# Kernel tuning notes

Hardware: AMD Instinct MI355X
Metric: run time of the kernel (lower is better)

The kernel has to match this reference:

```python
import jax, jax.numpy as jnp
import numpy as np

B, C, OUT, K, H, W = 16, 128, 128, 3, 128, 128
EPS = 1e-5


def setup_inputs() -> dict:
    key = jax.random.key(0)
    ks = jax.random.split(key, 16)
    s = 0.05  # weight init scale to keep activations tame
    d = {
        "ir_feat": jax.random.normal(ks[0], (B, C, H, W), jnp.float32),
        "vi_feat": jax.random.normal(ks[1], (B, C, H, W), jnp.float32),
        # kernel_gen: 1x1 convs on pooled [B,2C,1,1] -> matmuls
        "kg_w1": jax.random.normal(ks[2], (C // 2, 2 * C), jnp.float32) * s,
        "kg_b1": jax.random.normal(ks[3], (C // 2,), jnp.float32) * s,
        "kg_w2": jax.random.normal(ks[4], (OUT * C * K * K, C // 2), jnp.float32) * s,
        "kg_b2": jax.random.normal(ks[5], (OUT * C * K * K,), jnp.float32) * s,
        # bias_gen
        "bg_w1": jax.random.normal(ks[6], (C // 4, 2 * C), jnp.float32) * s,
        "bg_b1": jax.random.normal(ks[7], (C // 4,), jnp.float32) * s,
        "bg_w2": jax.random.normal(ks[8], (OUT, C // 4), jnp.float32) * s,
        "bg_b2": jax.random.normal(ks[9], (OUT,), jnp.float32) * s,
        # enhance: 1x1 conv (no bias) + BN (eval-mode running stats)
        "en_w": jax.random.normal(ks[10], (C, 2 * C), jnp.float32) * s,
        "bn_gamma": jnp.ones((C,), jnp.float32),
        "bn_beta": jnp.zeros((C,), jnp.float32),
        "bn_mean": jax.random.normal(ks[11], (C,), jnp.float32) * 0.1,
        "bn_var": jax.random.uniform(ks[12], (C,), jnp.float32, 0.5, 1.5),
    }
    return d


def reference(ir_feat, vi_feat, kg_w1, kg_b1, kg_w2, kg_b2,
              bg_w1, bg_b1, bg_w2, bg_b2, en_w,
              bn_gamma, bn_beta, bn_mean, bn_var):
    concat = jnp.concatenate([ir_feat, vi_feat], axis=1)        # [B,2C,H,W]
    pooled = concat.mean(axis=(2, 3))                            # AdaptiveAvgPool2d(1) -> [B,2C]

    # dynamic kernel generation (1x1 convs on 1x1 spatial == matmuls)
    hk = jax.nn.relu(pooled @ kg_w1.T + kg_b1)                   # [B,C/2]
    dyn_k = (hk @ kg_w2.T + kg_b2).reshape(B, OUT, C, K, K)      # per-sample conv weights
    hb = jax.nn.relu(pooled @ bg_w1.T + bg_b1)                   # [B,C/4]
    dyn_b = hb @ bg_w2.T + bg_b2                                 # [B,OUT]

    # enhance: 1x1 conv -> BN(eval) -> ReLU
    enh = jnp.einsum('bchw,oc->bohw', concat, en_w)              # [B,C,H,W]
    inv = (bn_gamma / jnp.sqrt(bn_var + EPS))[:, None, None]
    enh = jax.nn.relu(enh * inv + (bn_beta - bn_mean * bn_gamma / jnp.sqrt(bn_var + EPS))[:, None, None])

    # per-sample dynamic conv2d, batched via vmap (replaces the python loop)
    def conv_one(x, w, b):  # x:[C,H,W], w:[OUT,C,K,K], b:[OUT]
        y = jax.lax.conv_general_dilated(
            x[None], w, window_strides=(1, 1), padding=[(1, 1), (1, 1)],
            dimension_numbers=('NCHW', 'OIHW', 'NCHW'))[0]
        return y + b[:, None, None]

    return jax.vmap(conv_one)(enh, dyn_k, dyn_b)                 # [B,OUT,H,W]
```

## Files before the change

kernel.cpp:

```cpp
#include <hip/hip_runtime.h>
#include <hip/hip_bf16.h>

#define B_    16
#define C_    128
#define TWOC  256
#define OUT_  128
#define HW    16384
#define WDIM  128
#define HDIM  128
#define KTOT  1152

typedef __attribute__((ext_vector_type(8))) short short8;
typedef __attribute__((ext_vector_type(4))) float floatx4;

__device__ __forceinline__ ushort f2bf(float f) {
    union { float f; uint u; } x; x.f = f;
    uint r = (x.u + 0x7FFFu + ((x.u >> 16) & 1u)) >> 16;
    return (ushort)r;
}
__device__ __forceinline__ float bf2f(ushort u) {
    union { float f; uint u; } x; x.u = ((uint)u) << 16;
    return x.f;
}
__device__ __forceinline__ uint cvt_pk_bf16(float lo, float hi) {
    uint r;
    asm("v_cvt_pk_bf16_f32 %0, %1, %2" : "=v"(r) : "v"(lo), "v"(hi));
    return r;
}

__global__ __launch_bounds__(256) void prep_kernel(
    const float* __restrict__ en_w, ushort* __restrict__ en_w_bf,
    float* __restrict__ pooled)
{
    int i = blockIdx.x * 256 + threadIdx.x;
    en_w_bf[i] = f2bf(en_w[i]);
    if (i < B_ * TWOC) pooled[i] = 0.f;
}

__global__ __launch_bounds__(256) void enhance_kernel(
    const float* __restrict__ ir, const float* __restrict__ vi,
    const ushort* __restrict__ en_w_bf,
    const float* __restrict__ gamma, const float* __restrict__ beta,
    const float* __restrict__ mean, const float* __restrict__ var,
    ushort* __restrict__ enh, float* __restrict__ pooled)
{
    __shared__ ushort Xs[128][40];
    __shared__ float red[256];
    const int b = blockIdx.y;
    const int p0 = blockIdx.x * 128;
    const int t = threadIdx.x;
    const int lane = t & 63, wave = t >> 6;
    const int wr = wave >> 1, wc = wave & 1;
    const int lr = lane & 15, kg = lane >> 4;
    const int px = t & 127, half = t >> 7;
    const int pc = t & 31, grp = t >> 5;

    floatx4 acc[4][4] = {};
    float fcur[16], fnxt[16];
    short8 a_cur[4], a_nxt[4];

    {
        const float* src = ir + ((size_t)b * C_ + half * 16) * HW + p0 + px;
        #pragma unroll
        for (int jj = 0; jj < 16; ++jj) fcur[jj] = src[(size_t)jj * HW];
        #pragma unroll
        for (int i2 = 0; i2 < 4; ++i2) {
            int co = wr * 64 + i2 * 16 + lr;
            a_cur[i2] = *(const short8*)&en_w_bf[(size_t)co * TWOC + kg * 8];
        }
    }

    #pragma unroll
    for (int kc = 0; kc < 8; ++kc) {
        __syncthreads();
        {
            uint u[8];
            #pragma unroll
            for (int jj = 0; jj < 8; ++jj)
                u[jj] = cvt_pk_bf16(fcur[2 * jj], fcur[2 * jj + 1]);
            uint4* dst = (uint4*)&Xs[px][half * 16];
            dst[0] = make_uint4(u[0], u[1], u[2], u[3]);
            dst[1] = make_uint4(u[4], u[5], u[6], u[7]);
        }
        if (kc > 0 && t < 32) {
            float s = red[t] + red[32 + t] + red[64 + t] + red[96 + t]
                    + red[128 + t] + red[160 + t] + red[192 + t] + red[224 + t];
            atomicAdd(&pooled[b * TWOC + (kc - 1) * 32 + t], s);
        }
        __syncthreads();

        if (kc < 7) {
            int c2b = (kc + 1) * 32 + half * 16;
            const float* src = (c2b < C_)
                ? ir + ((size_t)b * C_ + c2b) * HW + p0 + px
                : vi + ((size_t)b * C_ + (c2b - C_)) * HW + p0 + px;
            #pragma unroll
            for (int jj = 0; jj < 16; ++jj) fnxt[jj] = src[(size_t)jj * HW];
            #pragma unroll
            for (int i2 = 0; i2 < 4; ++i2) {
                int co = wr * 64 + i2 * 16 + lr;
                a_nxt[i2] = *(const short8*)&en_w_bf[(size_t)co * TWOC + (kc + 1) * 32 + kg * 8];
            }
        }

        short8 bfr[4];
        #pragma unroll
        for (int j = 0; j < 4; ++j) {
            int pl = wc * 64 + j * 16 + lr;
            bfr[j] = *(const short8*)&Xs[pl][kg * 8];
        }
        #pragma unroll
        for (int i2 = 0; i2 < 4; ++i2)
            #pragma unroll
            for (int j = 0; j < 4; ++j)
                acc[i2][j] = __builtin_amdgcn_mfma_f32_16x16x32_bf16(a_cur[i2], bfr[j], acc[i2][j], 0, 0, 0);

        {
            float s = 0.f;
            #pragma unroll
            for (int q = 0; q < 16; ++q) s += bf2f(Xs[grp * 16 + q][pc]);
            red[t] = s;
        }

        if (kc < 7) {
            #pragma unroll
            for (int jj = 0; jj < 16; ++jj) fcur[jj] = fnxt[jj];
            #pragma unroll
            for (int i2 = 0; i2 < 4; ++i2) a_cur[i2] = a_nxt[i2];
        }
    }

    __syncthreads();
    if (t < 32) {
        float s = red[t] + red[32 + t] + red[64 + t] + red[96 + t]
                + red[128 + t] + red[160 + t] + red[192 + t] + red[224 + t];
        atomicAdd(&pooled[b * TWOC + 7 * 32 + t], s);
    }

    #pragma unroll
    for (int i2 = 0; i2 < 4; ++i2) {
        int co_b = wr * 64 + i2 * 16 + kg * 4;
        float4 g  = *(const float4*)&gamma[co_b];
        float4 vv = *(const float4*)&var[co_b];
        float4 bt = *(const float4*)&beta[co_b];
        float4 mn = *(const float4*)&mean[co_b];
        float inv0 = g.x * rsqrtf(vv.x + 1e-5f), inv1 = g.y * rsqrtf(vv.y + 1e-5f);
        float inv2 = g.z * rsqrtf(vv.z + 1e-5f), inv3 = g.w * rsqrtf(vv.w + 1e-5f);
        float ad0 = bt.x - mn.x * inv0, ad1 = bt.y - mn.y * inv1;
        float ad2 = bt.z - mn.z * inv2, ad3 = bt.w - mn.w * inv3;
        #pragma unroll
        for (int j = 0; j < 4; ++j) {
            int pl = wc * 64 + j * 16 + lr;
            float v0 = fmaxf(acc[i2][j][0] * inv0 + ad0, 0.f);
            float v1 = fmaxf(acc[i2][j][1] * inv1 + ad1, 0.f);
            float v2 = fmaxf(acc[i2][j][2] * inv2 + ad2, 0.f);
            float v3 = fmaxf(acc[i2][j][3] * inv3 + ad3, 0.f);
            uint2 pk;
            pk.x = cvt_pk_bf16(v0, v1);
            pk.y = cvt_pk_bf16(v2, v3);
            *(uint2*)&enh[((size_t)b * HW + p0 + pl) * C_ + co_b] = pk;
        }
    }
}

__global__ __launch_bounds__(256) void gen_mlp1_kernel(
    const float* __restrict__ pooled,
    const float* __restrict__ kg_w1, const float* __restrict__ kg_b1,
    const float* __restrict__ bg_w1, const float* __restrict__ bg_b1,
    float* __restrict__ hk, float* __restrict__ hb)
{
    const float scale = 1.0f / (float)HW;
    int idx = blockIdx.x * 256 + threadIdx.x;
    if (idx < B_ * 64) {
        int b = idx >> 6, j = idx & 63;
        const float4* w = (const float4*)(kg_w1 + (size_t)j * TWOC);
        const float4* p = (const float4*)(pooled + b * TWOC);
        float s = 0.f;
        #pragma unroll 8
        for (int q = 0; q < 64; ++q) {
            float4 wv = w[q], pv = p[q];
            s += (wv.x * pv.x + wv.y * pv.y) + (wv.z * pv.z + wv.w * pv.w);
        }
        hk[idx] = fmaxf(kg_b1[j] + s * scale, 0.f);
    } else if (idx < B_ * 64 + B_ * 32) {
        int e = idx - B_ * 64;
        int b = e >> 5, j = e & 31;
        const float4* w = (const float4*)(bg_w1 + (size_t)j * TWOC);
        const float4* p = (const float4*)(pooled + b * TWOC);
        float s = 0.f;
        #pragma unroll 8
        for (int q = 0; q < 64; ++q) {
            float4 wv = w[q], pv = p[q];
            s += (wv.x * pv.x + wv.y * pv.y) + (wv.z * pv.z + wv.w * pv.w);
        }
        hb[e] = fmaxf(bg_b1[j] + s * scale, 0.f);
    }
}

__global__ __launch_bounds__(256) void gen_dynk_kernel(
    const float* __restrict__ kg_w2, const float* __restrict__ kg_b2,
    const float* __restrict__ hk, const float* __restrict__ hb,
    const float* __restrict__ bg_w2, const float* __restrict__ bg_b2,
    ushort* __restrict__ dynk, float* __restrict__ dyn_b)
{
    __shared__ float hk_s[B_][64];
    int t = threadIdx.x;
    for (int i = t; i < B_ * 64; i += 256) hk_s[i >> 6][i & 63] = hk[i];
    __syncthreads();

    int i = blockIdx.x * 256 + t;
    int kk = i >> 14;
    int o  = (i >> 7) & 127;
    int c  = i & 127;
    int r  = o * KTOT + c * 9 + kk;

    float wrow[64];
    const float4* w4 = (const float4*)(kg_w2 + (size_t)r * 64);
    #pragma unroll
    for (int q = 0; q < 16; ++q) {
        float4 v = w4[q];
        wrow[4 * q + 0] = v.x; wrow[4 * q + 1] = v.y;
        wrow[4 * q + 2] = v.z; wrow[4 * q + 3] = v.w;
    }
    float bias = kg_b2[r];
    #pragma unroll
    for (int b = 0; b < B_; ++b) {
        float s = bias;
        #pragma unroll
        for (int k2 = 0; k2 < 64; ++k2) s += hk_s[b][k2] * wrow[k2];
        dynk[((size_t)(b * 9 + kk) * 128 + o) * 128 + c] = f2bf(s);
    }

    if (blockIdx.x == 0) {
        for (int e = t; e < B_ * OUT_; e += 256) {
            int b = e >> 7, o2 = e & 127;
            float s = bg_b2[o2];
            const float* w = bg_w2 + o2 * 32;
            const float* h = hb + b * 32;
            #pragma unroll
            for (int k2 = 0; k2 < 32; ++k2) s += h[k2] * w[k2];
            dyn_b[e] = s;
        }
    }
}

__global__ __launch_bounds__(256, 3) void dynconv_kernel(
    const ushort* __restrict__ enh, const ushort* __restrict__ dynk,
    const float* __restrict__ dyn_b, float* __restrict__ out)
{
    __shared__ ushort halo[180][72];
    const int b = blockIdx.z;
    const int gy0 = blockIdx.y * 8, gx0 = blockIdx.x * 16;
    const int t = threadIdx.x, lane = t & 63, wave = t >> 6;
    const int wr = wave >> 1, wc = wave & 1;
    const int lr = lane & 15, kg = lane >> 4;
    const ushort* dynk_b = dynk + (size_t)b * 9 * 128 * 128;
    const ushort* enh_b  = enh + (size_t)b * HW * C_;

    floatx4 acc[4][4] = {};
    short8 a_cur[8], a_nxt[8];

    for (int h = 0; h < 2; ++h) {
        uint4 hreg[6];
        #pragma unroll
        for (int s = 0; s < 6; ++s) {
            int seg = s * 256 + t;
            int hp = seg >> 3, c8 = seg & 7;
            uint4 v = make_uint4(0, 0, 0, 0);
            if (hp < 180) {
                int hy = hp / 18, hx = hp - hy * 18;
                int gy = gy0 - 1 + hy, gx = gx0 - 1 + hx;
                if ((unsigned)gy < 128u && (unsigned)gx < 128u)
                    v = *(const uint4*)&enh_b[((size_t)(gy * WDIM + gx)) * C_ + h * 64 + c8 * 8];
            }
            hreg[s] = v;
        }
        #pragma unroll
        for (int q = 0; q < 8; ++q) {
            int ks = q >> 2, i2 = q & 3;
            int o = wr * 64 + i2 * 16 + lr;
            a_cur[q] = *(const short8*)&dynk_b[(size_t)(0 * 128 + o) * 128 + h * 64 + ks * 32 + kg * 8];
        }
        __syncthreads();
        #pragma unroll
        for (int s = 0; s < 6; ++s) {
            int seg = s * 256 + t;
            int hp = seg >> 3, c8 = seg & 7;
            if (hp < 180) *(uint4*)&halo[hp][c8 * 8] = hreg[s];
        }
        __syncthreads();

        #pragma unroll
        for (int kk = 0; kk < 9; ++kk) {
            if (kk < 8) {
                #pragma unroll
                for (int q = 0; q < 8; ++q) {
                    int ks = q >> 2, i2 = q & 3;
                    int o = wr * 64 + i2 * 16 + lr;
                    a_nxt[q] = *(const short8*)&dynk_b[(size_t)((kk + 1) * 128 + o) * 128 + h * 64 + ks * 32 + kg * 8];
                }
            }
            const int kh = kk / 3, kw = kk - kh * 3;
            #pragma unroll
            for (int ks = 0; ks < 2; ++ks) {
                short8 bfr[4];
                #pragma unroll
                for (int j = 0; j < 4; ++j) {
                    int p = wc * 64 + j * 16 + lr;
                    int py = p >> 4, px = p & 15;
                    bfr[j] = *(const short8*)&halo[(py + kh) * 18 + (px + kw)][ks * 32 + kg * 8];
                }
                #pragma unroll
                for (int i2 = 0; i2 < 4; ++i2)
                    #pragma unroll
                    for (int j = 0; j < 4; ++j)
                        acc[i2][j] = __builtin_amdgcn_mfma_f32_16x16x32_bf16(a_cur[ks * 4 + i2], bfr[j], acc[i2][j], 0, 0, 0);
            }
            #pragma unroll
            for (int q = 0; q < 8; ++q) a_cur[q] = a_nxt[q];
        }
    }

    #pragma unroll
    for (int i2 = 0; i2 < 4; ++i2) {
        int o_b = wr * 64 + i2 * 16 + kg * 4;
        float4 db = *(const float4*)&dyn_b[b * OUT_ + o_b];
        float dbv[4] = {db.x, db.y, db.z, db.w};
        #pragma unroll
        for (int j = 0; j < 4; ++j) {
            int p = wc * 64 + j * 16 + lr;
            int py = p >> 4, px = p & 15;
            int gy = gy0 + py, gx = gx0 + px;
            #pragma unroll
            for (int r = 0; r < 4; ++r) {
                int o = o_b + r;
                out[((size_t)(b * OUT_ + o)) * HW + gy * WDIM + gx] = acc[i2][j][r] + dbv[r];
            }
        }
    }
}

extern "C" void kernel_launch(void* const* d_in, const int* in_sizes, int n_in,
                              void* d_out, int out_size, void* d_ws, size_t ws_size,
                              hipStream_t stream)
{
    const float* ir    = (const float*)d_in[0];
    const float* vi    = (const float*)d_in[1];
    const float* kg_w1 = (const float*)d_in[2];
    const float* kg_b1 = (const float*)d_in[3];
    const float* kg_w2 = (const float*)d_in[4];
    const float* kg_b2 = (const float*)d_in[5];
    const float* bg_w1 = (const float*)d_in[6];
    const float* bg_b1 = (const float*)d_in[7];
    const float* bg_w2 = (const float*)d_in[8];
    const float* bg_b2 = (const float*)d_in[9];
    const float* en_w  = (const float*)d_in[10];
    const float* bn_g  = (const float*)d_in[11];
    const float* bn_b  = (const float*)d_in[12];
    const float* bn_m  = (const float*)d_in[13];
    const float* bn_v  = (const float*)d_in[14];
    float* out = (float*)d_out;

    char* ws = (char*)d_ws;
    float*  pooled = (float*)(ws + 0);
    float*  dyn_b  = (float*)(ws + 16384);
    float*  hk     = (float*)(ws + 24576);
    float*  hb     = (float*)(ws + 28672);
    ushort* dynk   = (ushort*)(ws + 32768);
    ushort* enh    = (ushort*)(ws + 32768 + 4718592);

    size_t en_off = 32768 + 4718592 + 67108864;
    ushort* en_w_bf = (ws_size >= en_off + 65536)
                    ? (ushort*)(ws + en_off)
                    : (ushort*)((char*)d_out + (size_t)out_size - 65536);

    prep_kernel<<<128, 256, 0, stream>>>(en_w, en_w_bf, pooled);
    enhance_kernel<<<dim3(HDIM, B_), 256, 0, stream>>>(ir, vi, en_w_bf, bn_g, bn_b,
                                                       bn_m, bn_v, enh, pooled);
    gen_mlp1_kernel<<<6, 256, 0, stream>>>(pooled, kg_w1, kg_b1, bg_w1, bg_b1, hk, hb);
    gen_dynk_kernel<<<576, 256, 0, stream>>>(kg_w2, kg_b2, hk, hb, bg_w2, bg_b2, dynk, dyn_b);
    dynconv_kernel<<<dim3(WDIM / 16, HDIM / 8, B_), 256, 0, stream>>>(enh, dynk, dyn_b, out);
}
```

Measured before the change: 590.5 us.

## Retile dynamic conv into 4x32 pixel tiles, split output channels across blocks

Changes the dynamic-conv tiling from 8x16 pixels times 128 outputs per block to 4x32 pixels times 64 outputs, so each wave handles one row of 32 pixels. The grid becomes a flat 4096 blocks with an XCD-aware swizzle that groups blocks of the same batch together, and occupancy is raised to 4 blocks per CU by halving the accumulators. The output stores now cover 32 contiguous x-positions per wave, which should coalesce better. In exchange, each halo tile is loaded twice, once for each output half, and weight fragments are reused over fewer pixels.

```diff
diff --git a/kernel.cpp b/kernel.cpp
--- a/kernel.cpp
+++ b/kernel.cpp
@@ -244,31 +244,42 @@
     }
 }
 
-__global__ __launch_bounds__(256, 3) void dynconv_kernel(
+#define TY_   4
+#define TX_   32
+#define HX_   34
+#define NPX_  204
+
+__global__ __launch_bounds__(256, 4) void dynconv_kernel(
     const ushort* __restrict__ enh, const ushort* __restrict__ dynk,
     const float* __restrict__ dyn_b, float* __restrict__ out)
 {
-    __shared__ ushort halo[180][72];
-    const int b = blockIdx.z;
-    const int gy0 = blockIdx.y * 8, gx0 = blockIdx.x * 16;
-    const int t = threadIdx.x, lane = t & 63, wave = t >> 6;
-    const int wr = wave >> 1, wc = wave & 1;
+    __shared__ ushort halo[NPX_][72];
+    const int pid = blockIdx.x;
+    const int lid = (pid & 7) * 512 + (pid >> 3);
+    const int b   = lid >> 8;
+    const int rem = lid & 255;
+    const int oh  = rem & 1;
+    const int tile = rem >> 1;
+    const int ty = tile >> 2, tx = tile & 3;
+    const int gy0 = ty * TY_, gx0 = tx * TX_;
+
+    const int t = threadIdx.x, lane = t & 63, wc = t >> 6;
     const int lr = lane & 15, kg = lane >> 4;
     const ushort* dynk_b = dynk + (size_t)b * 9 * 128 * 128;
     const ushort* enh_b  = enh + (size_t)b * HW * C_;
 
-    floatx4 acc[4][4] = {};
+    floatx4 acc[4][2] = {};
     short8 a_cur[8], a_nxt[8];
 
     for (int h = 0; h < 2; ++h) {
-        uint4 hreg[6];
-        #pragma unroll
-        for (int s = 0; s < 6; ++s) {
+        uint4 hreg[7];
+        #pragma unroll
+        for (int s = 0; s < 7; ++s) {
             int seg = s * 256 + t;
             int hp = seg >> 3, c8 = seg & 7;
             uint4 v = make_uint4(0, 0, 0, 0);
-            if (hp < 180) {
-                int hy = hp / 18, hx = hp - hy * 18;
+            if (hp < NPX_) {
+                int hy = hp / HX_, hx = hp - hy * HX_;
                 int gy = gy0 - 1 + hy, gx = gx0 - 1 + hx;
                 if ((unsigned)gy < 128u && (unsigned)gx < 128u)
                     v = *(const uint4*)&enh_b[((size_t)(gy * WDIM + gx)) * C_ + h * 64 + c8 * 8];
@@ -278,15 +289,15 @@
         #pragma unroll
         for (int q = 0; q < 8; ++q) {
             int ks = q >> 2, i2 = q & 3;
-            int o = wr * 64 + i2 * 16 + lr;
+            int o = oh * 64 + i2 * 16 + lr;
             a_cur[q] = *(const short8*)&dynk_b[(size_t)(0 * 128 + o) * 128 + h * 64 + ks * 32 + kg * 8];
         }
         __syncthreads();
         #pragma unroll
-        for (int s = 0; s < 6; ++s) {
+        for (int s = 0; s < 7; ++s) {
             int seg = s * 256 + t;
             int hp = seg >> 3, c8 = seg & 7;
-            if (hp < 180) *(uint4*)&halo[hp][c8 * 8] = hreg[s];
+            if (hp < NPX_) *(uint4*)&halo[hp][c8 * 8] = hreg[s];
         }
         __syncthreads();
 
@@ -296,24 +307,21 @@
                 #pragma unroll
                 for (int q = 0; q < 8; ++q) {
                     int ks = q >> 2, i2 = q & 3;
-                    int o = wr * 64 + i2 * 16 + lr;
+                    int o = oh * 64 + i2 * 16 + lr;
                     a_nxt[q] = *(const short8*)&dynk_b[(size_t)((kk + 1) * 128 + o) * 128 + h * 64 + ks * 32 + kg * 8];
                 }
             }
             const int kh = kk / 3, kw = kk - kh * 3;
             #pragma unroll
             for (int ks = 0; ks < 2; ++ks) {
-                short8 bfr[4];
+                short8 bfr[2];
                 #pragma unroll
-                for (int j = 0; j < 4; ++j) {
-                    int p = wc * 64 + j * 16 + lr;
-                    int py = p >> 4, px = p & 15;
-                    bfr[j] = *(const short8*)&halo[(py + kh) * 18 + (px + kw)][ks * 32 + kg * 8];
-                }
+                for (int j = 0; j < 2; ++j)
+                    bfr[j] = *(const short8*)&halo[(wc + kh) * HX_ + j * 16 + lr + kw][ks * 32 + kg * 8];
                 #pragma unroll
                 for (int i2 = 0; i2 < 4; ++i2)
                     #pragma unroll
-                    for (int j = 0; j < 4; ++j)
+                    for (int j = 0; j < 2; ++j)
                         acc[i2][j] = __builtin_amdgcn_mfma_f32_16x16x32_bf16(a_cur[ks * 4 + i2], bfr[j], acc[i2][j], 0, 0, 0);
             }
             #pragma unroll
@@ -321,16 +329,15 @@
         }
     }
 
+    const int gy = gy0 + wc;
     #pragma unroll
     for (int i2 = 0; i2 < 4; ++i2) {
-        int o_b = wr * 64 + i2 * 16 + kg * 4;
+        int o_b = oh * 64 + i2 * 16 + kg * 4;
         float4 db = *(const float4*)&dyn_b[b * OUT_ + o_b];
         float dbv[4] = {db.x, db.y, db.z, db.w};
         #pragma unroll
-        for (int j = 0; j < 4; ++j) {
-            int p = wc * 64 + j * 16 + lr;
-            int py = p >> 4, px = p & 15;
-            int gy = gy0 + py, gx = gx0 + px;
+        for (int j = 0; j < 2; ++j) {
+            int gx = gx0 + j * 16 + lr;
             #pragma unroll
             for (int r = 0; r < 4; ++r) {
                 int o = o_b + r;
@@ -379,5 +386,5 @@
                                                        bn_m, bn_v, enh, pooled);
     gen_mlp1_kernel<<<6, 256, 0, stream>>>(pooled, kg_w1, kg_b1, bg_w1, bg_b1, hk, hb);
     gen_dynk_kernel<<<576, 256, 0, stream>>>(kg_w2, kg_b2, hk, hb, bg_w2, bg_b2, dynk, dyn_b);
-    dynconv_kernel<<<dim3(WDIM / 16, HDIM / 8, B_), 256, 0, stream>>>(enh, dynk, dyn_b, out);
-}
+    dynconv_kernel<<<4096, 256, 0, stream>>>(enh, dynk, dyn_b, out);
+}
```

After: 664.8 us. +12.6%, slower.
